# Optimization experiments

Measured on AMD Instinct MI355X. Metric: run time of the kernel, lower is better.

Reference implementation:

```python
import jax, jax.numpy as jnp
import numpy as np
import math

B, L, DIM, H = 1, 2048, 512, 8
D = DIM // H
STEPS = 1024
TWO_PI = 2.0 * math.pi
CHUNK = 64  # matches torch chunk_size


def setup_inputs() -> dict:
    key = jax.random.key(0)
    ks = jax.random.split(key, 6)
    x = jax.random.normal(ks[0], (B, L, DIM), jnp.float32)
    W_qs = jax.random.normal(ks[1], (DIM, 2 * DIM), jnp.float32) * 0.02
    b_qs = jnp.zeros((2 * DIM,), jnp.float32)
    ln_w = jnp.ones((2 * DIM,), jnp.float32)
    ln_b = jnp.zeros((2 * DIM,), jnp.float32)
    freq = jax.random.normal(ks[2], (H,), jnp.float32) * 0.02
    phase_shift = jax.random.normal(ks[3], (H,), jnp.float32) * 0.02
    W_out = jax.random.normal(ks[4], (DIM, DIM), jnp.float32) * 0.02
    b_out = jnp.zeros((DIM,), jnp.float32)
    # buffer: cos(linspace(0, 2pi, 1024)) exactly as in _init_lookup_tables
    cos_table = jnp.cos(jnp.linspace(0.0, TWO_PI, STEPS)).astype(jnp.float32)
    return dict(x=x, W_qs=W_qs, b_qs=b_qs, ln_w=ln_w, ln_b=ln_b,
                freq=freq, phase_shift=phase_shift, W_out=W_out, b_out=b_out,
                cos_table=cos_table)


def _forward(x, W_qs, b_qs, ln_w, ln_b, freq, phase_shift, W_out, b_out, cos_table):
    # quantum state preparation (shared module applied to same x => q == k states)
    qs = x @ W_qs + b_qs                                  # [B,L,2*DIM]
    mu = jnp.mean(qs, axis=-1, keepdims=True)
    var = jnp.var(qs, axis=-1, keepdims=True)
    qs = (qs - mu) / jnp.sqrt(var + 1e-5) * ln_w + ln_b    # LayerNorm(2*dim)
    amp, phase = jnp.split(qs, 2, axis=-1)                 # [B,L,DIM] each
    amp = jax.nn.sigmoid(amp)
    amp = amp / (jnp.sqrt(jnp.sum(amp ** 2, axis=-1, keepdims=True)) + 1e-8)
    phase = jnp.tanh(phase) * math.pi

    to_heads = lambda t: t.reshape(B, L, H, D).transpose(0, 2, 1, 3)  # [B,H,L,D]
    q_amp = to_heads(amp)
    q_phase = to_heads(phase)
    v = to_heads(x)

    NC = L // CHUNK
    qa_c = q_amp.reshape(B, H, NC, CHUNK, D).transpose(2, 0, 1, 3, 4)   # [NC,B,H,C,D]
    qp_c = q_phase.reshape(B, H, NC, CHUNK, D).transpose(2, 0, 1, 3, 4)
    f = freq[None, :, None, None, None]
    s = phase_shift[None, :, None, None, None]

    def chunk(carry, qc):
        qa, qp = qc                                         # [B,H,C,D]
        # pairwise per-dim phase interference via lookup table
        pd = (qp[:, :, :, None, :] - q_phase[:, :, None, :, :]) * f + s  # [B,H,C,L,D]
        idx = ((pd / TWO_PI * STEPS) % STEPS).astype(jnp.int32)
        interf = cos_table[idx]
        score = jnp.sum(qa[:, :, :, None, :] * q_amp[:, :, None, :, :] * interf,
                        axis=-1)                            # [B,H,C,L]
        return carry, score

    _, scores = jax.lax.scan(jax.checkpoint(chunk), 0, (qa_c, qp_c))
    scores = scores.transpose(1, 2, 0, 3, 4).reshape(B, H, L, L)
    attn = jax.nn.softmax(scores / math.sqrt(D), axis=-1)
    out = jnp.einsum('bhqk,bhkd->bhqd', attn, v)            # [B,H,L,D]
    out = out.transpose(0, 2, 1, 3).reshape(B, L, DIM)
    return out @ W_out + b_out


def reference(x, W_qs, b_qs, ln_w, ln_b, freq, phase_shift, W_out, b_out, cos_table):
    return _forward(x, W_qs, b_qs, ln_w, ln_b, freq, phase_shift, W_out, b_out, cos_table)
```

## Files before the change

kernel.cpp:

```cpp
#include <hip/hip_runtime.h>
#include <cstdint>
#include <cstddef>


typedef __attribute__((ext_vector_type(8))) short short8;
typedef __attribute__((ext_vector_type(4))) float f32x4;

#define MFMA16(a, b, c) __builtin_amdgcn_mfma_f32_16x16x32_bf16((a), (b), (c), 0, 0, 0)

static constexpr size_t B_QS   = 0;
static constexpr size_t B_ATTB = 0;
static constexpr size_t B_UB   = (size_t)8 * 1024 * 1024;
static constexpr size_t B_WB   = B_UB + (size_t)4 * 1024 * 1024;
static constexpr size_t B_XB   = B_WB + (size_t)4 * 1024 * 1024;
static constexpr size_t B_VT   = B_XB + (size_t)2 * 1024 * 1024;
static constexpr size_t B_WQT  = B_VT + (size_t)2 * 1024 * 1024;
static constexpr size_t B_WOT  = B_WQT + (size_t)1 * 1024 * 1024;

__device__ __forceinline__ unsigned short f2bf(float f) {
  unsigned u = __float_as_uint(f);
  return (unsigned short)((u + 0x7FFFu + ((u >> 16) & 1u)) >> 16);
}

__global__ __launch_bounds__(256) void k_prep(const float* __restrict__ x,
    const float* __restrict__ Wq, const float* __restrict__ Wo,
    unsigned short* __restrict__ xb, unsigned short* __restrict__ vT,
    unsigned short* __restrict__ WqT, unsigned short* __restrict__ WoT) {
  __shared__ float tl[64 * 65];
  const int t = threadIdx.x;
  const int b = blockIdx.x;
  if (b < 256) {
    const int i0 = (b >> 3) * 64, h = b & 7;
    #pragma unroll
    for (int it = 0; it < 16; ++it) {
      int n = t + 256 * it;
      int r = n >> 6, c = n & 63;
      float v = x[(size_t)(i0 + r) * 512 + h * 64 + c];
      tl[r * 65 + c] = v;
      xb[(size_t)(i0 + r) * 512 + h * 64 + c] = f2bf(v);
    }
    __syncthreads();
    #pragma unroll
    for (int it = 0; it < 16; ++it) {
      int n = t + 256 * it;
      int d = n >> 6, ii = n & 63;
      vT[(size_t)(h * 64 + d) * 2048 + i0 + ii] = f2bf(tl[ii * 65 + d]);
    }
  } else {
    int bb = b - 256;
    const float* src; unsigned short* dst; int k0, n0, N;
    if (bb < 128) { src = Wq; dst = WqT; k0 = (bb >> 4) * 64; n0 = (bb & 15) * 64; N = 1024; }
    else { bb -= 128; src = Wo; dst = WoT; k0 = (bb >> 3) * 64; n0 = (bb & 7) * 64; N = 512; }
    #pragma unroll
    for (int it = 0; it < 16; ++it) {
      int n = t + 256 * it;
      int r = n >> 6, c = n & 63;
      tl[r * 65 + c] = src[(size_t)(k0 + r) * N + n0 + c];
    }
    __syncthreads();
    #pragma unroll
    for (int it = 0; it < 16; ++it) {
      int n = t + 256 * it;
      int rr = n >> 6, cc = n & 63;
      dst[(size_t)(n0 + rr) * 512 + k0 + cc] = f2bf(tl[cc * 65 + rr]);
    }
  }
}

__global__ __launch_bounds__(256) void k_gemm(const unsigned short* __restrict__ A,
    const unsigned short* __restrict__ Bt, const float* __restrict__ bias,
    float* __restrict__ C, int N) {
  __shared__ __align__(16) unsigned char sm[2 * 64 * 136];
  unsigned char* s_a = sm;
  unsigned char* s_b = sm + 64 * 136;
  const int m0 = blockIdx.x * 64, n0 = blockIdx.y * 64;
  const int t = threadIdx.x;
  const int wave = t >> 6, lane = t & 63;
  const int m = lane & 15, quad = lane >> 4;
  const int sr = t >> 2, spart = t & 3;
  f32x4 acc[4] = {{0,0,0,0},{0,0,0,0},{0,0,0,0},{0,0,0,0}};
  for (int kc = 0; kc < 512; kc += 64) {
    #pragma unroll
    for (int it = 0; it < 2; ++it) {
      *(short8*)(s_a + sr * 136 + spart * 32 + it * 16) =
        *(const short8*)(A + (size_t)(m0 + sr) * 512 + kc + spart * 16 + it * 8);
      *(short8*)(s_b + sr * 136 + spart * 32 + it * 16) =
        *(const short8*)(Bt + (size_t)(n0 + sr) * 512 + kc + spart * 16 + it * 8);
    }
    __syncthreads();
    #pragma unroll
    for (int k2 = 0; k2 < 2; ++k2) {
      short8 af = *(const short8*)(s_a + (wave * 16 + m) * 136 + k2 * 64 + quad * 16);
      #pragma unroll
      for (int nt = 0; nt < 4; ++nt) {
        short8 bf = *(const short8*)(s_b + (nt * 16 + m) * 136 + k2 * 64 + quad * 16);
        acc[nt] = MFMA16(af, bf, acc[nt]);
      }
    }
    __syncthreads();
  }
  #pragma unroll
  for (int nt = 0; nt < 4; ++nt) {
    int col = n0 + nt * 16 + m;
    float bv = bias[col];
    #pragma unroll
    for (int r = 0; r < 4; ++r) {
      int row = m0 + wave * 16 + quad * 4 + r;
      C[(size_t)row * N + col] = acc[nt][r] + bv;
    }
  }
}

__global__ __launch_bounds__(256) void k_ln_act(const float* __restrict__ qs,
    const float* __restrict__ lnw, const float* __restrict__ lnb,
    const float* __restrict__ fr, const float* __restrict__ psh,
    unsigned short* __restrict__ Ub, unsigned short* __restrict__ Wb) {
  __shared__ float sred[12];
  const int i = blockIdx.x, t = threadIdx.x;
  const int wave = t >> 6, lane = t & 63;
  const float* row = qs + (size_t)i * 1024;
  float v0 = row[t], v1 = row[t + 256], v2 = row[t + 512], v3 = row[t + 768];
  float s = v0 + v1 + v2 + v3;
  float s2 = v0 * v0 + v1 * v1 + v2 * v2 + v3 * v3;
  #pragma unroll
  for (int off = 32; off; off >>= 1) {
    s += __shfl_down(s, off, 64);
    s2 += __shfl_down(s2, off, 64);
  }
  if (lane == 0) { sred[wave] = s; sred[4 + wave] = s2; }
  __syncthreads();
  s = sred[0] + sred[1] + sred[2] + sred[3];
  s2 = sred[4] + sred[5] + sred[6] + sred[7];
  float mu = s * (1.0f / 1024.0f);
  float var = s2 * (1.0f / 1024.0f) - mu * mu;
  float rstd = 1.0f / sqrtf(var + 1e-5f);
  float y0 = (v0 - mu) * rstd * lnw[t]       + lnb[t];
  float y1 = (v1 - mu) * rstd * lnw[t + 256] + lnb[t + 256];
  float y2 = (v2 - mu) * rstd * lnw[t + 512] + lnb[t + 512];
  float y3 = (v3 - mu) * rstd * lnw[t + 768] + lnb[t + 768];
  float a0 = __builtin_amdgcn_rcpf(1.0f + __expf(-y0));
  float a1 = __builtin_amdgcn_rcpf(1.0f + __expf(-y1));
  float na = a0 * a0 + a1 * a1;
  #pragma unroll
  for (int off = 32; off; off >>= 1) na += __shfl_down(na, off, 64);
  __syncthreads();
  if (lane == 0) sred[8 + wave] = na;
  __syncthreads();
  na = sred[8] + sred[9] + sred[10] + sred[11];
  float inv = 1.0f / (sqrtf(na) + 1e-8f);
  float af0 = a0 * inv, af1 = a1 * inv;
  const float PI_F = 3.14159265358979323846f;
  float e2a = __expf(2.0f * y2);
  float e2b = __expf(2.0f * y3);
  float p2 = (1.0f - 2.0f * __builtin_amdgcn_rcpf(e2a + 1.0f)) * PI_F;
  float p3 = (1.0f - 2.0f * __builtin_amdgcn_rcpf(e2b + 1.0f)) * PI_F;
  const double GAM = 1024.0 / 1023.0;
  int h0 = t >> 6, d0 = t & 63, h1 = h0 + 4;
  float c10 = (float)((double)fr[h0] * GAM);
  float s10 = (float)((double)psh[h0] * GAM);
  float c11 = (float)((double)fr[h1] * GAM);
  float s11 = (float)((double)psh[h1] * GAM);
  float A0 = fmaf(p2, c10, s10), Bp0 = p2 * c10;
  float A1 = fmaf(p3, c11, s11), Bp1 = p3 * c11;
  float cA0, sA0, cB0, sB0, cA1, sA1, cB1, sB1;
  __sincosf(A0, &sA0, &cA0);
  __sincosf(Bp0, &sB0, &cB0);
  __sincosf(A1, &sA1, &cA1);
  __sincosf(Bp1, &sB1, &cB1);
  size_t b0 = ((size_t)h0 * 2048 + i) * 128 + d0;
  size_t b1 = ((size_t)h1 * 2048 + i) * 128 + d0;
  Ub[b0] = f2bf(af0 * cA0);  Ub[b0 + 64] = f2bf(af0 * sA0);
  Wb[b0] = f2bf(af0 * cB0);  Wb[b0 + 64] = f2bf(af0 * sB0);
  Ub[b1] = f2bf(af1 * cA1);  Ub[b1 + 64] = f2bf(af1 * sA1);
  Wb[b1] = f2bf(af1 * cB1);  Wb[b1 + 64] = f2bf(af1 * sB1);
}

__global__ __launch_bounds__(512, 2) void k_flash5(const unsigned short* __restrict__ Ub,
    const unsigned short* __restrict__ Wb, const unsigned short* __restrict__ vT,
    unsigned short* __restrict__ attb) {
  __shared__ __align__(16) unsigned char s_w[2][128 * 272];
  __shared__ __align__(16) unsigned char s_v[2][64 * 272];
  __shared__ __align__(16) unsigned char s_p[8][16 * 144];
  const int qt = blockIdx.x, h = blockIdx.y;
  const int q0 = qt * 64;
  const int t = threadIdx.x;
  const int wave = t >> 6, lane = t & 63;
  const int qw = wave & 3, kw = wave >> 2;
  const int m = lane & 15, quad = lane >> 4;
  const int sr = t >> 2, sp = t & 3;
  const int vr = t >> 3, vp = t & 7;
  unsigned char* s_pw = s_p[wave];
  short8 afr[4];
  const unsigned short* urow = Ub + ((size_t)h * 2048 + q0 + qw * 16 + m) * 128;
  #pragma unroll
  for (int fs = 0; fs < 4; ++fs)
    afr[fs] = *(const short8*)(urow + fs * 32 + quad * 8);
  short8 ones;
  #pragma unroll
  for (int j = 0; j < 8; ++j) ones[j] = (short)0x3F80;
  f32x4 oacc[4] = {{0,0,0,0},{0,0,0,0},{0,0,0,0},{0,0,0,0}};
  f32x4 dacc = {0, 0, 0, 0};
  const unsigned short* wgbase = Wb + (size_t)h * 2048 * 128 + (size_t)sr * 128;
  const unsigned short* vgbase = vT + ((size_t)h * 64 + vr) * 2048;
  #pragma unroll
  for (int it = 0; it < 4; ++it)
    *(short8*)(s_w[0] + sr * 272 + sp * 64 + it * 16) =
      *(const short8*)(wgbase + sp * 32 + it * 8);
  #pragma unroll
  for (int it = 0; it < 2; ++it)
    *(short8*)(s_v[0] + vr * 272 + vp * 32 + it * 16) =
      *(const short8*)(vgbase + vp * 16 + it * 8);
  __syncthreads();
  for (int kt = 0; kt < 16; ++kt) {
    const int cur = kt & 1;
    short8 wst[4], vst[2];
    const bool has = (kt < 15);
    if (has) {
      const unsigned short* wg = wgbase + (size_t)(kt + 1) * 128 * 128;
      #pragma unroll
      for (int it = 0; it < 4; ++it)
        wst[it] = *(const short8*)(wg + sp * 32 + it * 8);
      const unsigned short* vg = vgbase + (kt + 1) * 128;
      #pragma unroll
      for (int it = 0; it < 2; ++it)
        vst[it] = *(const short8*)(vg + vp * 16 + it * 8);
    }
    f32x4 sc[4] = {{0,0,0,0},{0,0,0,0},{0,0,0,0},{0,0,0,0}};
    #pragma unroll
    for (int ksub = 0; ksub < 4; ++ksub) {
      const int krow = kw * 64 + ksub * 16 + m;
      #pragma unroll
      for (int fs = 0; fs < 4; ++fs) {
        short8 bfr = *(const short8*)(s_w[cur] + krow * 272 + fs * 64 + quad * 16);
        sc[ksub] = MFMA16(afr[fs], bfr, sc[ksub]);
      }
    }
    #pragma unroll
    for (int ksub = 0; ksub < 4; ++ksub)
      #pragma unroll
      for (int r = 0; r < 4; ++r) {
        float p = __expf(sc[ksub][r] * 0.125f);
        *(unsigned short*)(s_pw + (quad * 4 + r) * 144 + (ksub * 16 + m) * 2) = f2bf(p);
      }
    if (has) {
      #pragma unroll
      for (int it = 0; it < 4; ++it)
        *(short8*)(s_w[cur ^ 1] + sr * 272 + sp * 64 + it * 16) = wst[it];
      #pragma unroll
      for (int it = 0; it < 2; ++it)
        *(short8*)(s_v[cur ^ 1] + vr * 272 + vp * 32 + it * 16) = vst[it];
    }
    __syncthreads();
    #pragma unroll
    for (int k2 = 0; k2 < 2; ++k2) {
      short8 pf = *(const short8*)(s_pw + m * 144 + k2 * 64 + quad * 16);
      dacc = MFMA16(pf, ones, dacc);
      #pragma unroll
      for (int dt = 0; dt < 4; ++dt) {
        short8 vf = *(const short8*)(s_v[cur] + (dt * 16 + m) * 272 +
                                     kw * 128 + k2 * 64 + quad * 16);
        oacc[dt] = MFMA16(pf, vf, oacc[dt]);
      }
    }
    __syncthreads();
  }
  float* s_ored = (float*)(s_w[0]);
  float* s_dred = (float*)(s_w[0] + 16384);
  if (kw == 1) {
    #pragma unroll
    for (int dt = 0; dt < 4; ++dt)
      #pragma unroll
      for (int r = 0; r < 4; ++r)
        s_ored[qw * 1024 + (quad * 4 + r) * 64 + dt * 16 + m] = oacc[dt][r];
    if (m == 0) {
      #pragma unroll
      for (int r = 0; r < 4; ++r)
        s_dred[qw * 16 + quad * 4 + r] = dacc[r];
    }
  }
  __syncthreads();
  if (kw == 0) {
    float invd[4];
    #pragma unroll
    for (int r = 0; r < 4; ++r)
      invd[r] = 1.0f / (dacc[r] + s_dred[qw * 16 + quad * 4 + r]);
    #pragma unroll
    for (int dt = 0; dt < 4; ++dt)
      #pragma unroll
      for (int r = 0; r < 4; ++r) {
        float o = oacc[dt][r] + s_ored[qw * 1024 + (quad * 4 + r) * 64 + dt * 16 + m];
        attb[(size_t)(q0 + qw * 16 + quad * 4 + r) * 512 + h * 64 + dt * 16 + m] =
            f2bf(o * invd[r]);
      }
  }
}

extern "C" void kernel_launch(void* const* d_in, const int* in_sizes, int n_in,
                              void* d_out, int out_size, void* d_ws, size_t ws_size,
                              hipStream_t stream) {
  (void)in_sizes; (void)n_in; (void)out_size; (void)ws_size;
  const float* x   = (const float*)d_in[0];
  const float* Wq  = (const float*)d_in[1];
  const float* bq  = (const float*)d_in[2];
  const float* lnw = (const float*)d_in[3];
  const float* lnb = (const float*)d_in[4];
  const float* fr  = (const float*)d_in[5];
  const float* ps  = (const float*)d_in[6];
  const float* Wo  = (const float*)d_in[7];
  const float* bo  = (const float*)d_in[8];
  char* ws = (char*)d_ws;
  float*          qs   = (float*)(ws + B_QS);
  unsigned short* attb = (unsigned short*)(ws + B_ATTB);
  unsigned short* Ub   = (unsigned short*)(ws + B_UB);
  unsigned short* Wb   = (unsigned short*)(ws + B_WB);
  unsigned short* xb   = (unsigned short*)(ws + B_XB);
  unsigned short* vT   = (unsigned short*)(ws + B_VT);
  unsigned short* WqT  = (unsigned short*)(ws + B_WQT);
  unsigned short* WoT  = (unsigned short*)(ws + B_WOT);
  float* out = (float*)d_out;

  k_prep<<<448, 256, 0, stream>>>(x, Wq, Wo, xb, vT, WqT, WoT);
  k_gemm<<<dim3(32, 16), 256, 0, stream>>>(xb, WqT, bq, qs, 1024);
  k_ln_act<<<2048, 256, 0, stream>>>(qs, lnw, lnb, fr, ps, Ub, Wb);
  k_flash5<<<dim3(32, 8), 512, 0, stream>>>(Ub, Wb, vT, attb);
  k_gemm<<<dim3(32, 8), 256, 0, stream>>>(attb, WoT, bo, out, 512);
}
```

Baseline: 156.0 us.

## Fuse QS projection GEMM with LayerNorm/activation and move next-tile LDS stores after PV

Replaces the separate x@Wq GEMM and LayerNorm/activation kernels with a single kernel. Each 512-thread block computes 16 full rows of qs in registers from an MFMA-fragment-packed WqT, then does the LayerNorm, sigmoid/tanh and sincos epilogue on-chip. This removes the fp32 qs round trip through global memory and one launch. The flash kernel also drops one __syncthreads per iteration by writing prefetched W/V tiles after the PV MFMAs. The trade-off is that the fused kernel launches only 128 blocks and streams B fragments straight from global memory.

```diff
diff --git a/kernel.cpp b/kernel.cpp
--- a/kernel.cpp
+++ b/kernel.cpp
@@ -8,12 +8,10 @@
 
 #define MFMA16(a, b, c) __builtin_amdgcn_mfma_f32_16x16x32_bf16((a), (b), (c), 0, 0, 0)
 
-static constexpr size_t B_QS   = 0;
 static constexpr size_t B_ATTB = 0;
-static constexpr size_t B_UB   = (size_t)8 * 1024 * 1024;
+static constexpr size_t B_UB   = (size_t)2 * 1024 * 1024;
 static constexpr size_t B_WB   = B_UB + (size_t)4 * 1024 * 1024;
-static constexpr size_t B_XB   = B_WB + (size_t)4 * 1024 * 1024;
-static constexpr size_t B_VT   = B_XB + (size_t)2 * 1024 * 1024;
+static constexpr size_t B_VT   = B_WB + (size_t)4 * 1024 * 1024;
 static constexpr size_t B_WQT  = B_VT + (size_t)2 * 1024 * 1024;
 static constexpr size_t B_WOT  = B_WQT + (size_t)1 * 1024 * 1024;
 
@@ -24,20 +22,17 @@
 
 __global__ __launch_bounds__(256) void k_prep(const float* __restrict__ x,
     const float* __restrict__ Wq, const float* __restrict__ Wo,
-    unsigned short* __restrict__ xb, unsigned short* __restrict__ vT,
-    unsigned short* __restrict__ WqT, unsigned short* __restrict__ WoT) {
+    unsigned short* __restrict__ vT, unsigned short* __restrict__ WqTp,
+    unsigned short* __restrict__ WoT) {
   __shared__ float tl[64 * 65];
-  const int t = threadIdx.x;
-  const int b = blockIdx.x;
+  const int t = threadIdx.x, b = blockIdx.x;
   if (b < 256) {
     const int i0 = (b >> 3) * 64, h = b & 7;
     #pragma unroll
     for (int it = 0; it < 16; ++it) {
       int n = t + 256 * it;
       int r = n >> 6, c = n & 63;
-      float v = x[(size_t)(i0 + r) * 512 + h * 64 + c];
-      tl[r * 65 + c] = v;
-      xb[(size_t)(i0 + r) * 512 + h * 64 + c] = f2bf(v);
+      tl[r * 65 + c] = x[(size_t)(i0 + r) * 512 + h * 64 + c];
     }
     __syncthreads();
     #pragma unroll
@@ -46,133 +41,207 @@
       int d = n >> 6, ii = n & 63;
       vT[(size_t)(h * 64 + d) * 2048 + i0 + ii] = f2bf(tl[ii * 65 + d]);
     }
+  } else if (b < 384) {
+    const int bb = b - 256;
+    const int k0 = (bb >> 4) * 64, n0 = (bb & 15) * 64;
+    #pragma unroll
+    for (int it = 0; it < 16; ++it) {
+      int n = t + 256 * it;
+      int r = n >> 6, c = n & 63;
+      tl[r * 65 + c] = Wq[(size_t)(k0 + r) * 1024 + n0 + c];
+    }
+    __syncthreads();
+    #pragma unroll
+    for (int it = 0; it < 16; ++it) {
+      int n = t + 256 * it;
+      int rr = n >> 6, cc = n & 63;
+      int nn = n0 + rr, kk = k0 + cc;
+      int nt = nn >> 4, mm = nn & 15;
+      int kc32 = kk >> 5, qd = (kk >> 3) & 3, j = kk & 7;
+      WqTp[(((size_t)nt * 16 + kc32) * 64 + qd * 16 + mm) * 8 + j] =
+          f2bf(tl[cc * 65 + rr]);
+    }
   } else {
-    int bb = b - 256;
-    const float* src; unsigned short* dst; int k0, n0, N;
-    if (bb < 128) { src = Wq; dst = WqT; k0 = (bb >> 4) * 64; n0 = (bb & 15) * 64; N = 1024; }
-    else { bb -= 128; src = Wo; dst = WoT; k0 = (bb >> 3) * 64; n0 = (bb & 7) * 64; N = 512; }
+    const int bb = b - 384;
+    const int k0 = (bb >> 3) * 64, n0 = (bb & 7) * 64;
     #pragma unroll
     for (int it = 0; it < 16; ++it) {
       int n = t + 256 * it;
       int r = n >> 6, c = n & 63;
-      tl[r * 65 + c] = src[(size_t)(k0 + r) * N + n0 + c];
+      tl[r * 65 + c] = Wo[(size_t)(k0 + r) * 512 + n0 + c];
     }
     __syncthreads();
     #pragma unroll
     for (int it = 0; it < 16; ++it) {
       int n = t + 256 * it;
       int rr = n >> 6, cc = n & 63;
-      dst[(size_t)(n0 + rr) * 512 + k0 + cc] = f2bf(tl[cc * 65 + rr]);
-    }
-  }
-}
-
-__global__ __launch_bounds__(256) void k_gemm(const unsigned short* __restrict__ A,
-    const unsigned short* __restrict__ Bt, const float* __restrict__ bias,
-    float* __restrict__ C, int N) {
-  __shared__ __align__(16) unsigned char sm[2 * 64 * 136];
-  unsigned char* s_a = sm;
-  unsigned char* s_b = sm + 64 * 136;
-  const int m0 = blockIdx.x * 64, n0 = blockIdx.y * 64;
-  const int t = threadIdx.x;
-  const int wave = t >> 6, lane = t & 63;
-  const int m = lane & 15, quad = lane >> 4;
-  const int sr = t >> 2, spart = t & 3;
-  f32x4 acc[4] = {{0,0,0,0},{0,0,0,0},{0,0,0,0},{0,0,0,0}};
-  for (int kc = 0; kc < 512; kc += 64) {
-    #pragma unroll
-    for (int it = 0; it < 2; ++it) {
-      *(short8*)(s_a + sr * 136 + spart * 32 + it * 16) =
-        *(const short8*)(A + (size_t)(m0 + sr) * 512 + kc + spart * 16 + it * 8);
-      *(short8*)(s_b + sr * 136 + spart * 32 + it * 16) =
-        *(const short8*)(Bt + (size_t)(n0 + sr) * 512 + kc + spart * 16 + it * 8);
-    }
-    __syncthreads();
-    #pragma unroll
-    for (int k2 = 0; k2 < 2; ++k2) {
-      short8 af = *(const short8*)(s_a + (wave * 16 + m) * 136 + k2 * 64 + quad * 16);
-      #pragma unroll
-      for (int nt = 0; nt < 4; ++nt) {
-        short8 bf = *(const short8*)(s_b + (nt * 16 + m) * 136 + k2 * 64 + quad * 16);
-        acc[nt] = MFMA16(af, bf, acc[nt]);
-      }
-    }
-    __syncthreads();
-  }
-  #pragma unroll
-  for (int nt = 0; nt < 4; ++nt) {
-    int col = n0 + nt * 16 + m;
-    float bv = bias[col];
-    #pragma unroll
-    for (int r = 0; r < 4; ++r) {
-      int row = m0 + wave * 16 + quad * 4 + r;
-      C[(size_t)row * N + col] = acc[nt][r] + bv;
-    }
-  }
-}
-
-__global__ __launch_bounds__(256) void k_ln_act(const float* __restrict__ qs,
+      WoT[(size_t)(n0 + rr) * 512 + k0 + cc] = f2bf(tl[cc * 65 + rr]);
+    }
+  }
+}
+
+__global__ __launch_bounds__(512) void k_qs_ln(const float* __restrict__ x,
+    const unsigned short* __restrict__ WqTp, const float* __restrict__ bq,
     const float* __restrict__ lnw, const float* __restrict__ lnb,
     const float* __restrict__ fr, const float* __restrict__ psh,
     unsigned short* __restrict__ Ub, unsigned short* __restrict__ Wb) {
-  __shared__ float sred[12];
-  const int i = blockIdx.x, t = threadIdx.x;
-  const int wave = t >> 6, lane = t & 63;
-  const float* row = qs + (size_t)i * 1024;
-  float v0 = row[t], v1 = row[t + 256], v2 = row[t + 512], v3 = row[t + 768];
-  float s = v0 + v1 + v2 + v3;
-  float s2 = v0 * v0 + v1 * v1 + v2 * v2 + v3 * v3;
-  #pragma unroll
-  for (int off = 32; off; off >>= 1) {
-    s += __shfl_down(s, off, 64);
-    s2 += __shfl_down(s2, off, 64);
-  }
-  if (lane == 0) { sred[wave] = s; sred[4 + wave] = s2; }
+  __shared__ __align__(16) unsigned short s_a[16 * 520];
+  __shared__ float s_amp[16 * 516];
+  __shared__ float red[8 * 16 * 2];
+  __shared__ float red2[4 * 16];
+  const int r0 = blockIdx.x * 16, t = threadIdx.x;
+  const int w = t >> 6, lane = t & 63, m = lane & 15, quad = lane >> 4;
+  {
+    const int row = t >> 5, cs = (t & 31) * 16;
+    const float4* xr = (const float4*)(x + (size_t)(r0 + row) * 512 + cs);
+    unsigned short tmp[16];
+    #pragma unroll
+    for (int q4 = 0; q4 < 4; ++q4) {
+      float4 v = xr[q4];
+      tmp[q4 * 4 + 0] = f2bf(v.x); tmp[q4 * 4 + 1] = f2bf(v.y);
+      tmp[q4 * 4 + 2] = f2bf(v.z); tmp[q4 * 4 + 3] = f2bf(v.w);
+    }
+    *(short8*)(s_a + row * 520 + cs)     = *(short8*)(tmp);
+    *(short8*)(s_a + row * 520 + cs + 8) = *(short8*)(tmp + 8);
+  }
   __syncthreads();
-  s = sred[0] + sred[1] + sred[2] + sred[3];
-  s2 = sred[4] + sred[5] + sred[6] + sred[7];
-  float mu = s * (1.0f / 1024.0f);
-  float var = s2 * (1.0f / 1024.0f) - mu * mu;
-  float rstd = 1.0f / sqrtf(var + 1e-5f);
-  float y0 = (v0 - mu) * rstd * lnw[t]       + lnb[t];
-  float y1 = (v1 - mu) * rstd * lnw[t + 256] + lnb[t + 256];
-  float y2 = (v2 - mu) * rstd * lnw[t + 512] + lnb[t + 512];
-  float y3 = (v3 - mu) * rstd * lnw[t + 768] + lnb[t + 768];
-  float a0 = __builtin_amdgcn_rcpf(1.0f + __expf(-y0));
-  float a1 = __builtin_amdgcn_rcpf(1.0f + __expf(-y1));
-  float na = a0 * a0 + a1 * a1;
-  #pragma unroll
-  for (int off = 32; off; off >>= 1) na += __shfl_down(na, off, 64);
+  f32x4 acc[8] = {{0,0,0,0},{0,0,0,0},{0,0,0,0},{0,0,0,0},
+                  {0,0,0,0},{0,0,0,0},{0,0,0,0},{0,0,0,0}};
+  for (int kc32 = 0; kc32 < 16; ++kc32) {
+    short8 af = *(const short8*)(s_a + m * 520 + kc32 * 32 + quad * 8);
+    const unsigned short* bp =
+        WqTp + (((size_t)(w * 8) * 16 + kc32) * 64 + lane) * 8;
+    #pragma unroll
+    for (int nt = 0; nt < 8; ++nt) {
+      short8 bf = *(const short8*)(bp + (size_t)nt * 8192);
+      acc[nt] = MFMA16(af, bf, acc[nt]);
+    }
+  }
+  #pragma unroll
+  for (int nt = 0; nt < 8; ++nt) {
+    float bv = bq[w * 128 + nt * 16 + m];
+    #pragma unroll
+    for (int r = 0; r < 4; ++r) acc[nt][r] += bv;
+  }
+  float s1[4] = {0, 0, 0, 0}, s2[4] = {0, 0, 0, 0};
+  #pragma unroll
+  for (int r = 0; r < 4; ++r)
+    #pragma unroll
+    for (int nt = 0; nt < 8; ++nt) {
+      float v = acc[nt][r];
+      s1[r] += v; s2[r] += v * v;
+    }
+  #pragma unroll
+  for (int off = 1; off < 16; off <<= 1)
+    #pragma unroll
+    for (int r = 0; r < 4; ++r) {
+      s1[r] += __shfl_xor(s1[r], off, 64);
+      s2[r] += __shfl_xor(s2[r], off, 64);
+    }
+  if (m == 0)
+    #pragma unroll
+    for (int r = 0; r < 4; ++r) {
+      red[(w * 16 + quad * 4 + r) * 2]     = s1[r];
+      red[(w * 16 + quad * 4 + r) * 2 + 1] = s2[r];
+    }
   __syncthreads();
-  if (lane == 0) sred[8 + wave] = na;
-  __syncthreads();
-  na = sred[8] + sred[9] + sred[10] + sred[11];
-  float inv = 1.0f / (sqrtf(na) + 1e-8f);
-  float af0 = a0 * inv, af1 = a1 * inv;
+  float mu[4], rstd[4];
+  #pragma unroll
+  for (int r = 0; r < 4; ++r) {
+    int row = quad * 4 + r;
+    float S = 0, S2 = 0;
+    #pragma unroll
+    for (int wp = 0; wp < 8; ++wp) {
+      S  += red[(wp * 16 + row) * 2];
+      S2 += red[(wp * 16 + row) * 2 + 1];
+    }
+    mu[r] = S * (1.0f / 1024.0f);
+    float var = S2 * (1.0f / 1024.0f) - mu[r] * mu[r];
+    rstd[r] = 1.0f / sqrtf(var + 1e-5f);
+  }
+  float y[8][4];
+  #pragma unroll
+  for (int nt = 0; nt < 8; ++nt) {
+    int c = w * 128 + nt * 16 + m;
+    float gw = lnw[c], gb = lnb[c];
+    #pragma unroll
+    for (int r = 0; r < 4; ++r)
+      y[nt][r] = (acc[nt][r] - mu[r]) * rstd[r] * gw + gb;
+  }
   const float PI_F = 3.14159265358979323846f;
-  float e2a = __expf(2.0f * y2);
-  float e2b = __expf(2.0f * y3);
-  float p2 = (1.0f - 2.0f * __builtin_amdgcn_rcpf(e2a + 1.0f)) * PI_F;
-  float p3 = (1.0f - 2.0f * __builtin_amdgcn_rcpf(e2b + 1.0f)) * PI_F;
-  const double GAM = 1024.0 / 1023.0;
-  int h0 = t >> 6, d0 = t & 63, h1 = h0 + 4;
-  float c10 = (float)((double)fr[h0] * GAM);
-  float s10 = (float)((double)psh[h0] * GAM);
-  float c11 = (float)((double)fr[h1] * GAM);
-  float s11 = (float)((double)psh[h1] * GAM);
-  float A0 = fmaf(p2, c10, s10), Bp0 = p2 * c10;
-  float A1 = fmaf(p3, c11, s11), Bp1 = p3 * c11;
-  float cA0, sA0, cB0, sB0, cA1, sA1, cB1, sB1;
-  __sincosf(A0, &sA0, &cA0);
-  __sincosf(Bp0, &sB0, &cB0);
-  __sincosf(A1, &sA1, &cA1);
-  __sincosf(Bp1, &sB1, &cB1);
-  size_t b0 = ((size_t)h0 * 2048 + i) * 128 + d0;
-  size_t b1 = ((size_t)h1 * 2048 + i) * 128 + d0;
-  Ub[b0] = f2bf(af0 * cA0);  Ub[b0 + 64] = f2bf(af0 * sA0);
-  Wb[b0] = f2bf(af0 * cB0);  Wb[b0 + 64] = f2bf(af0 * sB0);
-  Ub[b1] = f2bf(af1 * cA1);  Ub[b1 + 64] = f2bf(af1 * sA1);
-  Wb[b1] = f2bf(af1 * cB1);  Wb[b1 + 64] = f2bf(af1 * sB1);
+  if (w < 4) {
+    float a[8][4];
+    float na[4] = {0, 0, 0, 0};
+    #pragma unroll
+    for (int nt = 0; nt < 8; ++nt)
+      #pragma unroll
+      for (int r = 0; r < 4; ++r) {
+        float v = __builtin_amdgcn_rcpf(1.0f + __expf(-y[nt][r]));
+        a[nt][r] = v;
+        na[r] += v * v;
+      }
+    #pragma unroll
+    for (int off = 1; off < 16; off <<= 1)
+      #pragma unroll
+      for (int r = 0; r < 4; ++r) na[r] += __shfl_xor(na[r], off, 64);
+    if (m == 0)
+      #pragma unroll
+      for (int r = 0; r < 4; ++r) red2[w * 16 + quad * 4 + r] = na[r];
+    __syncthreads();
+    float inv[4];
+    #pragma unroll
+    for (int r = 0; r < 4; ++r) {
+      int row = quad * 4 + r;
+      float N = red2[row] + red2[16 + row] + red2[32 + row] + red2[48 + row];
+      inv[r] = 1.0f / (sqrtf(N) + 1e-8f);
+    }
+    #pragma unroll
+    for (int nt = 0; nt < 8; ++nt)
+      #pragma unroll
+      for (int r = 0; r < 4; ++r)
+        s_amp[(quad * 4 + r) * 516 + w * 128 + nt * 16 + m] = a[nt][r] * inv[r];
+    __syncthreads();
+  } else {
+    float p[8][4];
+    #pragma unroll
+    for (int nt = 0; nt < 8; ++nt)
+      #pragma unroll
+      for (int r = 0; r < 4; ++r) {
+        float e2 = __expf(2.0f * y[nt][r]);
+        p[nt][r] = (1.0f - 2.0f * __builtin_amdgcn_rcpf(e2 + 1.0f)) * PI_F;
+      }
+    __syncthreads();
+    __syncthreads();
+    const double GAM = 1024.0 / 1023.0;
+    const int hbase = (w - 4) * 2;
+    float c1[2], s1g[2];
+    #pragma unroll
+    for (int hh = 0; hh < 2; ++hh) {
+      c1[hh]  = (float)((double)fr[hbase + hh] * GAM);
+      s1g[hh] = (float)((double)psh[hbase + hh] * GAM);
+    }
+    #pragma unroll
+    for (int nt = 0; nt < 8; ++nt) {
+      const int hh = nt >> 2;
+      const int pc = (w - 4) * 128 + nt * 16 + m;
+      const int d = pc & 63;
+      #pragma unroll
+      for (int r = 0; r < 4; ++r) {
+        const int i = r0 + quad * 4 + r;
+        float af = s_amp[(quad * 4 + r) * 516 + pc];
+        float A = fmaf(p[nt][r], c1[hh], s1g[hh]);
+        float Bp = p[nt][r] * c1[hh];
+        float cA, sA, cB, sB;
+        __sincosf(A, &sA, &cA);
+        __sincosf(Bp, &sB, &cB);
+        size_t base = ((size_t)(hbase + hh) * 2048 + i) * 128 + d;
+        Ub[base]      = f2bf(af * cA);
+        Ub[base + 64] = f2bf(af * sA);
+        Wb[base]      = f2bf(af * cB);
+        Wb[base + 64] = f2bf(af * sB);
+      }
+    }
+  }
 }
 
 __global__ __launch_bounds__(512, 2) void k_flash5(const unsigned short* __restrict__ Ub,
@@ -242,15 +311,6 @@
         float p = __expf(sc[ksub][r] * 0.125f);
         *(unsigned short*)(s_pw + (quad * 4 + r) * 144 + (ksub * 16 + m) * 2) = f2bf(p);
       }
-    if (has) {
-      #pragma unroll
-      for (int it = 0; it < 4; ++it)
-        *(short8*)(s_w[cur ^ 1] + sr * 272 + sp * 64 + it * 16) = wst[it];
-      #pragma unroll
-      for (int it = 0; it < 2; ++it)
-        *(short8*)(s_v[cur ^ 1] + vr * 272 + vp * 32 + it * 16) = vst[it];
-    }
-    __syncthreads();
     #pragma unroll
     for (int k2 = 0; k2 < 2; ++k2) {
       short8 pf = *(const short8*)(s_pw + m * 144 + k2 * 64 + quad * 16);
@@ -262,6 +322,14 @@
         oacc[dt] = MFMA16(pf, vf, oacc[dt]);
       }
     }
+    if (has) {
+      #pragma unroll
+      for (int it = 0; it < 4; ++it)
+        *(short8*)(s_w[cur ^ 1] + sr * 272 + sp * 64 + it * 16) = wst[it];
+      #pragma unroll
+      for (int it = 0; it < 2; ++it)
+        *(short8*)(s_v[cur ^ 1] + vr * 272 + vp * 32 + it * 16) = vst[it];
+    }
     __syncthreads();
   }
   float* s_ored = (float*)(s_w[0]);
@@ -292,6 +360,50 @@
         attb[(size_t)(q0 + qw * 16 + quad * 4 + r) * 512 + h * 64 + dt * 16 + m] =
             f2bf(o * invd[r]);
       }
+  }
+}
+
+__global__ __launch_bounds__(256) void k_gemm(const unsigned short* __restrict__ A,
+    const unsigned short* __restrict__ Bt, const float* __restrict__ bias,
+    float* __restrict__ C, int N) {
+  __shared__ __align__(16) unsigned char sm[2 * 64 * 136];
+  unsigned char* s_a = sm;
+  unsigned char* s_b = sm + 64 * 136;
+  const int m0 = blockIdx.x * 64, n0 = blockIdx.y * 64;
+  const int t = threadIdx.x;
+  const int wave = t >> 6, lane = t & 63;
+  const int m = lane & 15, quad = lane >> 4;
+  const int sr = t >> 2, spart = t & 3;
+  f32x4 acc[4] = {{0,0,0,0},{0,0,0,0},{0,0,0,0},{0,0,0,0}};
+  for (int kc = 0; kc < 512; kc += 64) {
+    #pragma unroll
+    for (int it = 0; it < 2; ++it) {
+      *(short8*)(s_a + sr * 136 + spart * 32 + it * 16) =
+        *(const short8*)(A + (size_t)(m0 + sr) * 512 + kc + spart * 16 + it * 8);
+      *(short8*)(s_b + sr * 136 + spart * 32 + it * 16) =
+        *(const short8*)(Bt + (size_t)(n0 + sr) * 512 + kc + spart * 16 + it * 8);
+    }
+    __syncthreads();
+    #pragma unroll
+    for (int k2 = 0; k2 < 2; ++k2) {
+      short8 af = *(const short8*)(s_a + (wave * 16 + m) * 136 + k2 * 64 + quad * 16);
+      #pragma unroll
+      for (int nt = 0; nt < 4; ++nt) {
+        short8 bf = *(const short8*)(s_b + (nt * 16 + m) * 136 + k2 * 64 + quad * 16);
+        acc[nt] = MFMA16(af, bf, acc[nt]);
+      }
+    }
+    __syncthreads();
+  }
+  #pragma unroll
+  for (int nt = 0; nt < 4; ++nt) {
+    int col = n0 + nt * 16 + m;
+    float bv = bias[col];
+    #pragma unroll
+    for (int r = 0; r < 4; ++r) {
+      int row = m0 + wave * 16 + quad * 4 + r;
+      C[(size_t)row * N + col] = acc[nt][r] + bv;
+    }
   }
 }
 
@@ -309,19 +421,16 @@
   const float* Wo  = (const float*)d_in[7];
   const float* bo  = (const float*)d_in[8];
   char* ws = (char*)d_ws;
-  float*          qs   = (float*)(ws + B_QS);
   unsigned short* attb = (unsigned short*)(ws + B_ATTB);
   unsigned short* Ub   = (unsigned short*)(ws + B_UB);
   unsigned short* Wb   = (unsigned short*)(ws + B_WB);
-  unsigned short* xb   = (unsigned short*)(ws + B_XB);
   unsigned short* vT   = (unsigned short*)(ws + B_VT);
-  unsigned short* WqT  = (unsigned short*)(ws + B_WQT);
+  unsigned short* WqTp = (unsigned short*)(ws + B_WQT);
   unsigned short* WoT  = (unsigned short*)(ws + B_WOT);
   float* out = (float*)d_out;
 
-  k_prep<<<448, 256, 0, stream>>>(x, Wq, Wo, xb, vT, WqT, WoT);
-  k_gemm<<<dim3(32, 16), 256, 0, stream>>>(xb, WqT, bq, qs, 1024);
-  k_ln_act<<<2048, 256, 0, stream>>>(qs, lnw, lnb, fr, ps, Ub, Wb);
+  k_prep<<<448, 256, 0, stream>>>(x, Wq, Wo, vT, WqTp, WoT);
+  k_qs_ln<<<128, 512, 0, stream>>>(x, WqTp, bq, lnw, lnb, fr, ps, Ub, Wb);
   k_flash5<<<dim3(32, 8), 512, 0, stream>>>(Ub, Wb, vT, attb);
   k_gemm<<<dim3(32, 8), 256, 0, stream>>>(attb, WoT, bo, out, 512);
 }
```

Measured after the change: 150.6 us. 1.04x faster.

## Repartition flash kernel waves by key columns and output dims, drop cross-wave reduction

Applied to the files above, without the earlier changes.

The attention kernel now has each wave compute scores for all 64 queries against its own 16-key slice, reusing each loaded W fragment across four query groups. P is written to a shared double-buffered tile, and the PV product is split so that each wave owns a query group and half of the output dimensions over the full key tile. This removes the final shared-memory reduction between key-split waves and one barrier per iteration. In exchange, each wave holds more A fragments in registers and the launch bounds drop to one block per SM, which may reduce occupancy.

```diff
diff --git a/kernel.cpp b/kernel.cpp
--- a/kernel.cpp
+++ b/kernel.cpp
@@ -27,8 +27,7 @@
     unsigned short* __restrict__ xb, unsigned short* __restrict__ vT,
     unsigned short* __restrict__ WqT, unsigned short* __restrict__ WoT) {
   __shared__ float tl[64 * 65];
-  const int t = threadIdx.x;
-  const int b = blockIdx.x;
+  const int t = threadIdx.x, b = blockIdx.x;
   if (b < 256) {
     const int i0 = (b >> 3) * 64, h = b & 7;
     #pragma unroll
@@ -46,23 +45,37 @@
       int d = n >> 6, ii = n & 63;
       vT[(size_t)(h * 64 + d) * 2048 + i0 + ii] = f2bf(tl[ii * 65 + d]);
     }
+  } else if (b < 384) {
+    const int bb = b - 256;
+    const int k0 = (bb >> 4) * 64, n0 = (bb & 15) * 64;
+    #pragma unroll
+    for (int it = 0; it < 16; ++it) {
+      int n = t + 256 * it;
+      int r = n >> 6, c = n & 63;
+      tl[r * 65 + c] = Wq[(size_t)(k0 + r) * 1024 + n0 + c];
+    }
+    __syncthreads();
+    #pragma unroll
+    for (int it = 0; it < 16; ++it) {
+      int n = t + 256 * it;
+      int rr = n >> 6, cc = n & 63;
+      WqT[(size_t)(n0 + rr) * 512 + k0 + cc] = f2bf(tl[cc * 65 + rr]);
+    }
   } else {
-    int bb = b - 256;
-    const float* src; unsigned short* dst; int k0, n0, N;
-    if (bb < 128) { src = Wq; dst = WqT; k0 = (bb >> 4) * 64; n0 = (bb & 15) * 64; N = 1024; }
-    else { bb -= 128; src = Wo; dst = WoT; k0 = (bb >> 3) * 64; n0 = (bb & 7) * 64; N = 512; }
+    const int bb = b - 384;
+    const int k0 = (bb >> 3) * 64, n0 = (bb & 7) * 64;
     #pragma unroll
     for (int it = 0; it < 16; ++it) {
       int n = t + 256 * it;
       int r = n >> 6, c = n & 63;
-      tl[r * 65 + c] = src[(size_t)(k0 + r) * N + n0 + c];
+      tl[r * 65 + c] = Wo[(size_t)(k0 + r) * 512 + n0 + c];
     }
     __syncthreads();
     #pragma unroll
     for (int it = 0; it < 16; ++it) {
       int n = t + 256 * it;
       int rr = n >> 6, cc = n & 63;
-      dst[(size_t)(n0 + rr) * 512 + k0 + cc] = f2bf(tl[cc * 65 + rr]);
+      WoT[(size_t)(n0 + rr) * 512 + k0 + cc] = f2bf(tl[cc * 65 + rr]);
     }
   }
 }
@@ -175,30 +188,32 @@
   Wb[b1] = f2bf(af1 * cB1);  Wb[b1 + 64] = f2bf(af1 * sB1);
 }
 
-__global__ __launch_bounds__(512, 2) void k_flash5(const unsigned short* __restrict__ Ub,
+__global__ __launch_bounds__(512, 1) void k_flash6(const unsigned short* __restrict__ Ub,
     const unsigned short* __restrict__ Wb, const unsigned short* __restrict__ vT,
     unsigned short* __restrict__ attb) {
   __shared__ __align__(16) unsigned char s_w[2][128 * 272];
   __shared__ __align__(16) unsigned char s_v[2][64 * 272];
-  __shared__ __align__(16) unsigned char s_p[8][16 * 144];
+  __shared__ __align__(16) unsigned char s_p[2][64 * 272];
   const int qt = blockIdx.x, h = blockIdx.y;
   const int q0 = qt * 64;
   const int t = threadIdx.x;
   const int wave = t >> 6, lane = t & 63;
-  const int qw = wave & 3, kw = wave >> 2;
+  const int qg = wave & 3, dh = wave >> 2;
   const int m = lane & 15, quad = lane >> 4;
   const int sr = t >> 2, sp = t & 3;
   const int vr = t >> 3, vp = t & 7;
-  unsigned char* s_pw = s_p[wave];
-  short8 afr[4];
-  const unsigned short* urow = Ub + ((size_t)h * 2048 + q0 + qw * 16 + m) * 128;
-  #pragma unroll
-  for (int fs = 0; fs < 4; ++fs)
-    afr[fs] = *(const short8*)(urow + fs * 32 + quad * 8);
+  short8 afr[4][4];
+  #pragma unroll
+  for (int g = 0; g < 4; ++g) {
+    const unsigned short* urow = Ub + ((size_t)h * 2048 + q0 + g * 16 + m) * 128;
+    #pragma unroll
+    for (int fs = 0; fs < 4; ++fs)
+      afr[g][fs] = *(const short8*)(urow + fs * 32 + quad * 8);
+  }
   short8 ones;
   #pragma unroll
   for (int j = 0; j < 8; ++j) ones[j] = (short)0x3F80;
-  f32x4 oacc[4] = {{0,0,0,0},{0,0,0,0},{0,0,0,0},{0,0,0,0}};
+  f32x4 oacc[2] = {{0,0,0,0},{0,0,0,0}};
   f32x4 dacc = {0, 0, 0, 0};
   const unsigned short* wgbase = Wb + (size_t)h * 2048 * 128 + (size_t)sr * 128;
   const unsigned short* vgbase = vT + ((size_t)h * 64 + vr) * 2048;
@@ -227,21 +242,27 @@
     }
     f32x4 sc[4] = {{0,0,0,0},{0,0,0,0},{0,0,0,0},{0,0,0,0}};
     #pragma unroll
-    for (int ksub = 0; ksub < 4; ++ksub) {
-      const int krow = kw * 64 + ksub * 16 + m;
-      #pragma unroll
-      for (int fs = 0; fs < 4; ++fs) {
-        short8 bfr = *(const short8*)(s_w[cur] + krow * 272 + fs * 64 + quad * 16);
-        sc[ksub] = MFMA16(afr[fs], bfr, sc[ksub]);
+    for (int fs = 0; fs < 4; ++fs) {
+      short8 bfr = *(const short8*)(s_w[cur] + (wave * 16 + m) * 272 + fs * 64 + quad * 16);
+      #pragma unroll
+      for (int g = 0; g < 4; ++g)
+        sc[g] = MFMA16(afr[g][fs], bfr, sc[g]);
+    }
+    #pragma unroll
+    for (int g = 0; g < 4; ++g)
+      #pragma unroll
+      for (int r = 0; r < 4; ++r) {
+        float p = __expf(sc[g][r] * 0.125f);
+        *(unsigned short*)(s_p[cur] + (g * 16 + quad * 4 + r) * 272 +
+                           (wave * 16 + m) * 2) = f2bf(p);
       }
-    }
-    #pragma unroll
-    for (int ksub = 0; ksub < 4; ++ksub)
-      #pragma unroll
-      for (int r = 0; r < 4; ++r) {
-        float p = __expf(sc[ksub][r] * 0.125f);
-        *(unsigned short*)(s_pw + (quad * 4 + r) * 144 + (ksub * 16 + m) * 2) = f2bf(p);
-      }
+    short8 vf[4][2];
+    #pragma unroll
+    for (int k2 = 0; k2 < 4; ++k2)
+      #pragma unroll
+      for (int dt = 0; dt < 2; ++dt)
+        vf[k2][dt] = *(const short8*)(s_v[cur] + (dh * 32 + dt * 16 + m) * 272 +
+                                      k2 * 64 + quad * 16);
     if (has) {
       #pragma unroll
       for (int it = 0; it < 4; ++it)
@@ -252,47 +273,23 @@
     }
     __syncthreads();
     #pragma unroll
-    for (int k2 = 0; k2 < 2; ++k2) {
-      short8 pf = *(const short8*)(s_pw + m * 144 + k2 * 64 + quad * 16);
+    for (int k2 = 0; k2 < 4; ++k2) {
+      short8 pf = *(const short8*)(s_p[cur] + (qg * 16 + m) * 272 + k2 * 64 + quad * 16);
       dacc = MFMA16(pf, ones, dacc);
       #pragma unroll
-      for (int dt = 0; dt < 4; ++dt) {
-        short8 vf = *(const short8*)(s_v[cur] + (dt * 16 + m) * 272 +
-                                     kw * 128 + k2 * 64 + quad * 16);
-        oacc[dt] = MFMA16(pf, vf, oacc[dt]);
-      }
-    }
-    __syncthreads();
-  }
-  float* s_ored = (float*)(s_w[0]);
-  float* s_dred = (float*)(s_w[0] + 16384);
-  if (kw == 1) {
-    #pragma unroll
-    for (int dt = 0; dt < 4; ++dt)
-      #pragma unroll
-      for (int r = 0; r < 4; ++r)
-        s_ored[qw * 1024 + (quad * 4 + r) * 64 + dt * 16 + m] = oacc[dt][r];
-    if (m == 0) {
-      #pragma unroll
-      for (int r = 0; r < 4; ++r)
-        s_dred[qw * 16 + quad * 4 + r] = dacc[r];
-    }
-  }
-  __syncthreads();
-  if (kw == 0) {
-    float invd[4];
+      for (int dt = 0; dt < 2; ++dt)
+        oacc[dt] = MFMA16(pf, vf[k2][dt], oacc[dt]);
+    }
+  }
+  float invd[4];
+  #pragma unroll
+  for (int r = 0; r < 4; ++r) invd[r] = 1.0f / dacc[r];
+  #pragma unroll
+  for (int dt = 0; dt < 2; ++dt)
     #pragma unroll
     for (int r = 0; r < 4; ++r)
-      invd[r] = 1.0f / (dacc[r] + s_dred[qw * 16 + quad * 4 + r]);
-    #pragma unroll
-    for (int dt = 0; dt < 4; ++dt)
-      #pragma unroll
-      for (int r = 0; r < 4; ++r) {
-        float o = oacc[dt][r] + s_ored[qw * 1024 + (quad * 4 + r) * 64 + dt * 16 + m];
-        attb[(size_t)(q0 + qw * 16 + quad * 4 + r) * 512 + h * 64 + dt * 16 + m] =
-            f2bf(o * invd[r]);
-      }
-  }
+      attb[(size_t)(q0 + qg * 16 + quad * 4 + r) * 512 + h * 64 +
+           dh * 32 + dt * 16 + m] = f2bf(oacc[dt][r] * invd[r]);
 }
 
 extern "C" void kernel_launch(void* const* d_in, const int* in_sizes, int n_in,
@@ -322,6 +319,6 @@
   k_prep<<<448, 256, 0, stream>>>(x, Wq, Wo, xb, vT, WqT, WoT);
   k_gemm<<<dim3(32, 16), 256, 0, stream>>>(xb, WqT, bq, qs, 1024);
   k_ln_act<<<2048, 256, 0, stream>>>(qs, lnw, lnb, fr, ps, Ub, Wb);
-  k_flash5<<<dim3(32, 8), 512, 0, stream>>>(Ub, Wb, vT, attb);
+  k_flash6<<<dim3(32, 8), 512, 0, stream>>>(Ub, Wb, vT, attb);
   k_gemm<<<dim3(32, 8), 256, 0, stream>>>(attb, WoT, bo, out, 512);
 }
```

Result: no change. 153.5 us (-1.6%).
